# Kernel optimization log

Hardware: AMD Instinct MI355X
Metric: run time of the kernel (lower is better)

## Reference

```python
import jax, jax.numpy as jnp
import numpy as np

N_NODES = 50000
N_EDGES = 500000
IN_DIM = 64
OUT_DIM = 64
NUM_RELS = 16


def setup_inputs() -> dict:
    key = jax.random.key(0)
    ks = jax.random.split(key, 8)
    h = jax.random.normal(ks[0], (N_NODES, IN_DIM), dtype=jnp.float32)
    he = jax.random.normal(ks[1], (N_EDGES, IN_DIM), dtype=jnp.float32)
    src = jax.random.randint(ks[2], (N_EDGES,), 0, N_NODES)
    dst = jax.random.randint(ks[3], (N_EDGES,), 0, N_NODES)
    rel = jax.random.randint(ks[4], (N_EDGES,), 0, NUM_RELS)
    # xavier-ish scales
    W_shared = jax.random.normal(ks[5], (OUT_DIM, IN_DIM), dtype=jnp.float32) * (2.0 / (IN_DIM + OUT_DIM)) ** 0.5
    W_attn = jax.random.normal(ks[6], (1, 3 * OUT_DIM), dtype=jnp.float32) * (2.0 / (3 * OUT_DIM + 1)) ** 0.5
    W_rel = jax.random.normal(ks[7], (NUM_RELS, IN_DIM, OUT_DIM), dtype=jnp.float32) * (2.0 / (IN_DIM + OUT_DIM)) ** 0.5
    return {"h": h, "he": he, "src": src, "dst": dst, "rel": rel,
            "W_shared": W_shared, "W_attn": W_attn, "W_rel": W_rel}


def reference(h, he, src, dst, rel, W_shared, W_attn, W_rel):
    # --- edge attention: a = attn_fc([z_src, z_edge, z_dst]) (raw linear score, no softmax in original) ---
    Z = h @ W_shared.T                      # [N, out] project all nodes once
    ze = he @ W_shared.T                    # [E, out]
    # split attn weight to avoid materializing [E, 3*out] concat
    Wa_s, Wa_e, Wa_d = jnp.split(W_attn, 3, axis=1)   # each [1, out]
    a = Z[src] @ Wa_s.T + ze @ Wa_e.T + Z[dst] @ Wa_d.T   # [E, 1]
    # --- message: msg = (h_src @ W_rel[rel]) * a ---
    # compute per-(node, relation) transform once [N, R, out], then gather per edge
    H_all = jnp.einsum('ni,rio->nro', h, W_rel)          # [N, R, out]
    msg = H_all[src, rel] * a                             # [E, out]
    # --- scatter-sum aggregation into destination nodes ---
    out = jax.ops.segment_sum(msg, dst, num_segments=N_NODES)  # [N, out]
    # apply_func: activation (relu), no bias
    return jax.nn.relu(out)
```

## Files before the change

kernel.cpp:

```cpp
#include <hip/hip_runtime.h>
#include <math.h>

#define N_NODES 50000
#define N_EDGES 500000
#define NUM_RELS 16
#define GH 64
#define SCAN_BLKS 196
#define AE_BLKS 1954

typedef _Float16 f16x8 __attribute__((ext_vector_type(8)));
typedef _Float16 f16x4 __attribute__((ext_vector_type(4)));
typedef float    f32x4 __attribute__((ext_vector_type(4)));


__global__ void kz(int* __restrict__ c1, int* __restrict__ cu1,
                   int* __restrict__ c2, int* __restrict__ cu2) {
    int i = blockIdx.x * 256 + threadIdx.x;
    if (i < NUM_RELS) { c1[i] = 0; cu1[i] = 0; }
    if (i < N_NODES)  { c2[i] = 0; cu2[i] = 0; }
}

__global__ __launch_bounds__(256) void k_node(
    const float* __restrict__ h,
    const float* __restrict__ W_shared, const float* __restrict__ W_attn,
    const int* __restrict__ dst, const int* __restrict__ rel,
    float* __restrict__ sn, float* __restrict__ dn,
    int* __restrict__ c1, int* __restrict__ c2,
    _Float16* __restrict__ h_hi, _Float16* __restrict__ h_lo) {
    __shared__ float sus[64], sud[64];
    __shared__ int hist[NUM_RELS];
    const int t = threadIdx.x, bid = blockIdx.x, nb = gridDim.x;
    if (t < 64) {
        float us = 0.f, ud = 0.f;
        for (int o = 0; o < 64; ++o) {
            float w = W_shared[o * 64 + t];
            us = fmaf(w, W_attn[o],       us);
            ud = fmaf(w, W_attn[128 + o], ud);
        }
        sus[t] = us; sud[t] = ud;
    }
    if (t < NUM_RELS) hist[t] = 0;
    __syncthreads();

    int n = bid * 256 + t;
    if (n < N_NODES) {
        const float* hp = h + (size_t)n * 64;
        float s = 0.f, d = 0.f;
#pragma unroll
        for (int i = 0; i < 64; i += 4) {
            float4 v = *(const float4*)(hp + i);
            s = fmaf(v.x, sus[i], s);     s = fmaf(v.y, sus[i + 1], s);
            s = fmaf(v.z, sus[i + 2], s); s = fmaf(v.w, sus[i + 3], s);
            d = fmaf(v.x, sud[i], d);     d = fmaf(v.y, sud[i + 1], d);
            d = fmaf(v.z, sud[i + 2], d); d = fmaf(v.w, sud[i + 3], d);
            f16x4 hi, lo;
            hi[0] = (_Float16)v.x; lo[0] = (_Float16)(v.x - (float)hi[0]);
            hi[1] = (_Float16)v.y; lo[1] = (_Float16)(v.y - (float)hi[1]);
            hi[2] = (_Float16)v.z; lo[2] = (_Float16)(v.z - (float)hi[2]);
            hi[3] = (_Float16)v.w; lo[3] = (_Float16)(v.w - (float)hi[3]);
            *(f16x4*)(h_hi + (size_t)n * 64 + i) = hi;
            *(f16x4*)(h_lo + (size_t)n * 64 + i) = lo;
        }
        sn[n] = s; dn[n] = d;
    }
    for (int e = bid * 256 + t; e < N_EDGES; e += nb * 256) {
        atomicAdd(&hist[rel[e]], 1);
        atomicAdd(&c2[dst[e]], 1);
    }
    __syncthreads();
    if (t < NUM_RELS && hist[t]) atomicAdd(&c1[t], hist[t]);
}

__global__ __launch_bounds__(256) void k_scan1(const int* __restrict__ c2,
                                               int* __restrict__ partial) {
    const int t = threadIdx.x, bid = blockIdx.x;
    const int lane = t & 63, wv = t >> 6;
    __shared__ int ws[4];
    int idx = bid * 256 + t;
    int s = (idx < N_NODES) ? c2[idx] : 0;
#pragma unroll
    for (int off = 32; off > 0; off >>= 1) s += __shfl_xor(s, off, 64);
    if (lane == 0) ws[wv] = s;
    __syncthreads();
    if (t == 0) partial[bid] = ws[0] + ws[1] + ws[2] + ws[3];
}

__global__ __launch_bounds__(256) void k_scan2(const int* __restrict__ partial,
                                               int* __restrict__ pbase,
                                               int* __restrict__ offs2,
                                               const int* __restrict__ c1,
                                               int* __restrict__ offs1) {
    const int t = threadIdx.x;
    const int lane = t & 63, wv = t >> 6;
    __shared__ int wsum[4];
    int v = (t < SCAN_BLKS) ? partial[t] : 0;
    int x = v;
#pragma unroll
    for (int off = 1; off < 64; off <<= 1) {
        int y = __shfl_up(x, off, 64);
        if (lane >= off) x += y;
    }
    if (lane == 63) wsum[wv] = x;
    __syncthreads();
    int wbase = 0;
#pragma unroll
    for (int j = 0; j < 4; ++j) if (j < wv) wbase += wsum[j];
    int excl = wbase + x - v;
    pbase[t] = excl;
    if (t == 255) offs2[N_NODES] = excl;
    if (t == 0) {
        int b = 0;
        for (int r = 0; r < NUM_RELS; ++r) { offs1[r] = b; b += c1[r]; }
        offs1[NUM_RELS] = b;
    }
}

__global__ __launch_bounds__(256) void k_scan3(int* __restrict__ c2,
                                               const int* __restrict__ pbase,
                                               int* __restrict__ offs2) {
    const int t = threadIdx.x, bid = blockIdx.x;
    const int lane = t & 63, wv = t >> 6;
    __shared__ int wsum[4];
    int idx = bid * 256 + t;
    int v = (idx < N_NODES) ? c2[idx] : 0;
    int x = v;
#pragma unroll
    for (int off = 1; off < 64; off <<= 1) {
        int y = __shfl_up(x, off, 64);
        if (lane >= off) x += y;
    }
    if (lane == 63) wsum[wv] = x;
    __syncthreads();
    int wbase = 0;
#pragma unroll
    for (int j = 0; j < 4; ++j) if (j < wv) wbase += wsum[j];
    if (idx < N_NODES) offs2[idx] = pbase[bid] + wbase + x - v;
    if (idx < 4096) c2[idx] = 0;
}

__global__ __launch_bounds__(256) void k_ae(
    const float4* __restrict__ he4,
    const int* __restrict__ src, const int* __restrict__ dst,
    const int* __restrict__ rel,
    const float* __restrict__ W_shared, const float* __restrict__ W_attn,
    const float* __restrict__ sn, const float* __restrict__ dn,
    const int* __restrict__ offs1, int* __restrict__ cur1p,
    const int* __restrict__ offs2, int* __restrict__ cursor2,
    int* __restrict__ srcs, float* __restrict__ aes, int* __restrict__ perm) {
    __shared__ float sve[64];
    __shared__ float sdot[256];
    __shared__ int hist[NUM_RELS], bbase[NUM_RELS], soffs[NUM_RELS];
    const int t = threadIdx.x;
    const int lane = t & 63;
    const int w = t >> 6;
    const int e = blockIdx.x * 256 + t;

    const size_t fb = ((size_t)blockIdx.x * 256 + (size_t)w * 64) * 16;
    const size_t fmax = (size_t)N_EDGES * 16 - 1;
    float4 v[16];
#pragma unroll
    for (int k = 0; k < 16; ++k) {
        size_t fi = fb + (size_t)k * 64 + lane;
        if (fi > fmax) fi = fmax;
        v[k] = he4[fi];
    }

    if (t < 64) {
        float ve = 0.f;
        for (int o = 0; o < 64; ++o)
            ve = fmaf(W_shared[o * 64 + t], W_attn[64 + o], ve);
        sve[t] = ve;
    }
    if (t < NUM_RELS) { hist[t] = 0; soffs[t] = offs1[t]; }
    const bool valid = (e < N_EDGES);
    int r = 0, s_ = 0, d_ = 0;
    float sdv = 0.f;
    if (valid) {
        s_ = src[e]; d_ = dst[e]; r = rel[e];
        sdv = sn[s_] + dn[d_];
    }
    __syncthreads();

    {
        float4 u = *(const float4*)(sve + 4 * (lane & 15));
#pragma unroll
        for (int k = 0; k < 16; ++k) {
            float p = v[k].x * u.x + v[k].y * u.y + v[k].z * u.z + v[k].w * u.w;
            p += __shfl_xor(p, 1, 64);
            p += __shfl_xor(p, 2, 64);
            p += __shfl_xor(p, 4, 64);
            p += __shfl_xor(p, 8, 64);
            if ((lane & 15) == 0) sdot[w * 64 + k * 4 + (lane >> 4)] = p;
        }
    }
    int lpos = 0; float aev = 0.f;
    if (valid) {
        aev = sdot[t] + sdv;
        lpos = atomicAdd(&hist[r], 1);
    }
    __syncthreads();
    if (t < NUM_RELS) bbase[t] = hist[t] ? atomicAdd(&cur1p[t << 8], hist[t]) : 0;
    __syncthreads();
    if (valid) {
        int p1 = soffs[r] + bbase[r] + lpos;
        srcs[p1] = s_; aes[p1] = aev;
        int p2 = offs2[d_] + atomicAdd(&cursor2[d_], 1);
        perm[p1] = p2;
    }
}

__global__ __launch_bounds__(256, 4) void k_msg(
    const _Float16* __restrict__ h_hi, const _Float16* __restrict__ h_lo,
    const float* __restrict__ W_rel, const int* __restrict__ offs1,
    const int* __restrict__ srcs, const float* __restrict__ aes,
    const int* __restrict__ perm, float* __restrict__ msg)
{
    const int t = threadIdx.x;
    const int lane = t & 63;
    const int quad = lane >> 4;
    const int col  = lane & 15;
    const int wib  = t >> 6;
    const int rh   = blockIdx.x & 31;
    const int r    = rh & 15;
    const int half = rh >> 4;
    const int g    = blockIdx.x >> 5;
    const int wr   = g * 4 + wib;

    const int begin = __builtin_amdgcn_readfirstlane(offs1[r]);
    const int end   = __builtin_amdgcn_readfirstlane(offs1[r + 1]);

    const float* Wb = W_rel + (size_t)r * 4096;
    f16x8 bh[2][2], bl[2][2];
#pragma unroll
    for (int kb = 0; kb < 2; ++kb)
#pragma unroll
        for (int n2 = 0; n2 < 2; ++n2)
#pragma unroll
            for (int j = 0; j < 8; ++j) {
                float w = Wb[(kb * 32 + quad * 8 + j) * 64 + (half * 2 + n2) * 16 + col];
                _Float16 hi = (_Float16)w;
                bh[kb][n2][j] = hi;
                bl[kb][n2][j] = (_Float16)(w - (float)hi);
            }

    for (int base = begin + wr * 16; base < end; base += 256 * 16) {
        int m16 = end - base; if (m16 > 16) m16 = 16;
        const int ridx = base + (col < m16 ? col : m16 - 1);
        const int   sv = srcs[ridx];
        const float av = (col < m16) ? aes[ridx] : 0.f;
        const int   pv = (col < m16) ? perm[ridx] : 0;

        const _Float16* ph = h_hi + (size_t)sv * 64 + quad * 8;
        const _Float16* pl = h_lo + (size_t)sv * 64 + quad * 8;
        f16x8 ah0 = *(const f16x8*)ph, ah1 = *(const f16x8*)(ph + 32);
        f16x8 al0 = *(const f16x8*)pl, al1 = *(const f16x8*)(pl + 32);

        f32x4 acc0 = {0.f, 0.f, 0.f, 0.f};
        f32x4 acc1 = {0.f, 0.f, 0.f, 0.f};
        acc0 = __builtin_amdgcn_mfma_f32_16x16x32_f16(ah0, bh[0][0], acc0, 0, 0, 0);
        acc1 = __builtin_amdgcn_mfma_f32_16x16x32_f16(ah0, bh[0][1], acc1, 0, 0, 0);
        acc0 = __builtin_amdgcn_mfma_f32_16x16x32_f16(ah0, bl[0][0], acc0, 0, 0, 0);
        acc1 = __builtin_amdgcn_mfma_f32_16x16x32_f16(ah0, bl[0][1], acc1, 0, 0, 0);
        acc0 = __builtin_amdgcn_mfma_f32_16x16x32_f16(al0, bh[0][0], acc0, 0, 0, 0);
        acc1 = __builtin_amdgcn_mfma_f32_16x16x32_f16(al0, bh[0][1], acc1, 0, 0, 0);
        acc0 = __builtin_amdgcn_mfma_f32_16x16x32_f16(ah1, bh[1][0], acc0, 0, 0, 0);
        acc1 = __builtin_amdgcn_mfma_f32_16x16x32_f16(ah1, bh[1][1], acc1, 0, 0, 0);
        acc0 = __builtin_amdgcn_mfma_f32_16x16x32_f16(ah1, bl[1][0], acc0, 0, 0, 0);
        acc1 = __builtin_amdgcn_mfma_f32_16x16x32_f16(ah1, bl[1][1], acc1, 0, 0, 0);
        acc0 = __builtin_amdgcn_mfma_f32_16x16x32_f16(al1, bh[1][0], acc0, 0, 0, 0);
        acc1 = __builtin_amdgcn_mfma_f32_16x16x32_f16(al1, bh[1][1], acc1, 0, 0, 0);

#pragma unroll
        for (int reg = 0; reg < 4; ++reg) {
            const int m = quad * 4 + reg;
            const float am = __shfl(av, m, 64);
            const int   pm = __shfl(pv, m, 64);
            if (m < m16) {
                float* op = msg + (size_t)pm * 64 + half * 32 + col;
                op[0]  = am * acc0[reg];
                op[16] = am * acc1[reg];
            }
        }
    }
}

__global__ __launch_bounds__(256) void k_out(
    const float* __restrict__ msg,
    const int* __restrict__ offs2, float* __restrict__ out)
{
    const int lane = threadIdx.x & 63;
    const int gw   = blockIdx.x * 4 + (threadIdx.x >> 6);
    const int nw   = gridDim.x * 4;
    for (int n = gw; n < N_NODES; n += nw) {
        const int qb = offs2[n], qe = offs2[n + 1];
        float s0 = 0.f, s1 = 0.f, s2 = 0.f, s3 = 0.f;
        int q = qb;
        for (; q + 4 <= qe; q += 4) {
            s0 += msg[(size_t)q * 64 + lane];
            s1 += msg[(size_t)(q + 1) * 64 + lane];
            s2 += msg[(size_t)(q + 2) * 64 + lane];
            s3 += msg[(size_t)(q + 3) * 64 + lane];
        }
        for (; q < qe; ++q)
            s0 += msg[(size_t)q * 64 + lane];
        float s = (s0 + s1) + (s2 + s3);
        out[(size_t)n * 64 + lane] = fmaxf(s, 0.f);
    }
}

extern "C" void kernel_launch(void* const* d_in, const int* in_sizes, int n_in,
                              void* d_out, int out_size, void* d_ws, size_t ws_size,
                              hipStream_t stream) {
    const float*  h        = (const float*)d_in[0];
    const float4* he4      = (const float4*)d_in[1];
    const int*    src      = (const int*)d_in[2];
    const int*    dst      = (const int*)d_in[3];
    const int*    rel      = (const int*)d_in[4];
    const float*  W_shared = (const float*)d_in[5];
    const float*  W_attn   = (const float*)d_in[6];
    const float*  W_rel    = (const float*)d_in[7];
    float*        out      = (float*)d_out;

    int*      counts1 = (int*)d_ws + 0;
    int*      cursor1 = (int*)d_ws + 16;
    int*      offs1   = (int*)d_ws + 32;
    int*      counts2 = (int*)d_ws + 64;
    int*      cursor2 = (int*)d_ws + 50064;
    int*      offs2   = (int*)d_ws + 100064;
    float*    sn      = (float*)d_ws + 150080;
    float*    dn      = (float*)d_ws + 200080;
    int*      srcs    = (int*)d_ws + 250080;
    float*    aes     = (float*)d_ws + 750080;
    int*      perm    = (int*)d_ws + 1250080;
    _Float16* h_hi    = (_Float16*)((int*)d_ws + 1750080);
    _Float16* h_lo    = (_Float16*)((int*)d_ws + 3350080);
    int*      partial = srcs;
    int*      pbase   = srcs + 256;
    float*    msg     = (float*)d_in[1];

    kz<<<(N_NODES + 255) / 256, 256, 0, stream>>>(counts1, cursor1, counts2, cursor2);
    k_node<<<196, 256, 0, stream>>>(h, W_shared, W_attn, dst, rel,
                                    sn, dn, counts1, counts2, h_hi, h_lo);
    k_scan1<<<SCAN_BLKS, 256, 0, stream>>>(counts2, partial);
    k_scan2<<<1, 256, 0, stream>>>(partial, pbase, offs2, counts1, offs1);
    k_scan3<<<SCAN_BLKS, 256, 0, stream>>>(counts2, pbase, offs2);
    k_ae<<<AE_BLKS, 256, 0, stream>>>(he4, src, dst, rel, W_shared, W_attn, sn, dn,
                                      offs1, counts2, offs2, cursor2, srcs, aes, perm);
    k_msg<<<32 * GH, 256, 0, stream>>>(h_hi, h_lo, W_rel, offs1, srcs, aes, perm, msg);
    k_out<<<2048, 256, 0, stream>>>(msg, offs2, out);
}
```

Baseline: 337.8 us.

## Store messages in fp16 in relation order and gather via inverse permutation

The message kernel now writes per-edge messages as fp16, contiguously in relation-sorted order, instead of scattering fp32 rows to destination-sorted slots. The edge kernel records an inverse permutation (destination slot to relation slot), and the output kernel gathers message rows through it with an 8-way unrolled accumulation. This halves message write and read traffic and makes the message-kernel stores coalesced, in exchange for random row gathers in the reduction. It also adds fp16 rounding error to each message before summation.

```diff
diff --git a/kernel.cpp b/kernel.cpp
--- a/kernel.cpp
+++ b/kernel.cpp
@@ -146,7 +146,7 @@
     const float* __restrict__ sn, const float* __restrict__ dn,
     const int* __restrict__ offs1, int* __restrict__ cur1p,
     const int* __restrict__ offs2, int* __restrict__ cursor2,
-    int* __restrict__ srcs, float* __restrict__ aes, int* __restrict__ perm) {
+    int* __restrict__ srcs, float* __restrict__ aes, int* __restrict__ iperm) {
     __shared__ float sve[64];
     __shared__ float sdot[256];
     __shared__ int hist[NUM_RELS], bbase[NUM_RELS], soffs[NUM_RELS];
@@ -205,7 +205,7 @@
         int p1 = soffs[r] + bbase[r] + lpos;
         srcs[p1] = s_; aes[p1] = aev;
         int p2 = offs2[d_] + atomicAdd(&cursor2[d_], 1);
-        perm[p1] = p2;
+        iperm[p2] = p1;
     }
 }
 
@@ -213,7 +213,7 @@
     const _Float16* __restrict__ h_hi, const _Float16* __restrict__ h_lo,
     const float* __restrict__ W_rel, const int* __restrict__ offs1,
     const int* __restrict__ srcs, const float* __restrict__ aes,
-    const int* __restrict__ perm, float* __restrict__ msg)
+    _Float16* __restrict__ msg)
 {
     const int t = threadIdx.x;
     const int lane = t & 63;
@@ -248,7 +248,6 @@
         const int ridx = base + (col < m16 ? col : m16 - 1);
         const int   sv = srcs[ridx];
         const float av = (col < m16) ? aes[ridx] : 0.f;
-        const int   pv = (col < m16) ? perm[ridx] : 0;
 
         const _Float16* ph = h_hi + (size_t)sv * 64 + quad * 8;
         const _Float16* pl = h_lo + (size_t)sv * 64 + quad * 8;
@@ -274,18 +273,17 @@
         for (int reg = 0; reg < 4; ++reg) {
             const int m = quad * 4 + reg;
             const float am = __shfl(av, m, 64);
-            const int   pm = __shfl(pv, m, 64);
             if (m < m16) {
-                float* op = msg + (size_t)pm * 64 + half * 32 + col;
-                op[0]  = am * acc0[reg];
-                op[16] = am * acc1[reg];
+                _Float16* op = msg + (size_t)(base + m) * 64 + half * 32 + col;
+                op[0]  = (_Float16)(am * acc0[reg]);
+                op[16] = (_Float16)(am * acc1[reg]);
             }
         }
     }
 }
 
 __global__ __launch_bounds__(256) void k_out(
-    const float* __restrict__ msg,
+    const _Float16* __restrict__ msg, const int* __restrict__ iperm,
     const int* __restrict__ offs2, float* __restrict__ out)
 {
     const int lane = threadIdx.x & 63;
@@ -294,16 +292,30 @@
     for (int n = gw; n < N_NODES; n += nw) {
         const int qb = offs2[n], qe = offs2[n + 1];
         float s0 = 0.f, s1 = 0.f, s2 = 0.f, s3 = 0.f;
+        float s4 = 0.f, s5 = 0.f, s6 = 0.f, s7 = 0.f;
         int q = qb;
-        for (; q + 4 <= qe; q += 4) {
-            s0 += msg[(size_t)q * 64 + lane];
-            s1 += msg[(size_t)(q + 1) * 64 + lane];
-            s2 += msg[(size_t)(q + 2) * 64 + lane];
-            s3 += msg[(size_t)(q + 3) * 64 + lane];
-        }
-        for (; q < qe; ++q)
-            s0 += msg[(size_t)q * 64 + lane];
-        float s = (s0 + s1) + (s2 + s3);
+        for (; q + 8 <= qe; q += 8) {
+            int p0 = iperm[q],     p1 = iperm[q + 1];
+            int p2 = iperm[q + 2], p3 = iperm[q + 3];
+            int p4 = iperm[q + 4], p5 = iperm[q + 5];
+            int p6 = iperm[q + 6], p7 = iperm[q + 7];
+            s0 += (float)msg[(size_t)p0 * 64 + lane];
+            s1 += (float)msg[(size_t)p1 * 64 + lane];
+            s2 += (float)msg[(size_t)p2 * 64 + lane];
+            s3 += (float)msg[(size_t)p3 * 64 + lane];
+            s4 += (float)msg[(size_t)p4 * 64 + lane];
+            s5 += (float)msg[(size_t)p5 * 64 + lane];
+            s6 += (float)msg[(size_t)p6 * 64 + lane];
+            s7 += (float)msg[(size_t)p7 * 64 + lane];
+        }
+        for (; q + 2 <= qe; q += 2) {
+            int p0 = iperm[q], p1 = iperm[q + 1];
+            s0 += (float)msg[(size_t)p0 * 64 + lane];
+            s1 += (float)msg[(size_t)p1 * 64 + lane];
+        }
+        if (q < qe)
+            s0 += (float)msg[(size_t)iperm[q] * 64 + lane];
+        float s = ((s0 + s1) + (s2 + s3)) + ((s4 + s5) + (s6 + s7));
         out[(size_t)n * 64 + lane] = fmaxf(s, 0.f);
     }
 }
@@ -331,12 +343,12 @@
     float*    dn      = (float*)d_ws + 200080;
     int*      srcs    = (int*)d_ws + 250080;
     float*    aes     = (float*)d_ws + 750080;
-    int*      perm    = (int*)d_ws + 1250080;
+    int*      iperm   = (int*)d_ws + 1250080;
     _Float16* h_hi    = (_Float16*)((int*)d_ws + 1750080);
     _Float16* h_lo    = (_Float16*)((int*)d_ws + 3350080);
     int*      partial = srcs;
     int*      pbase   = srcs + 256;
-    float*    msg     = (float*)d_in[1];
+    _Float16* msg     = (_Float16*)d_in[1];
 
     kz<<<(N_NODES + 255) / 256, 256, 0, stream>>>(counts1, cursor1, counts2, cursor2);
     k_node<<<196, 256, 0, stream>>>(h, W_shared, W_attn, dst, rel,
@@ -345,7 +357,7 @@
     k_scan2<<<1, 256, 0, stream>>>(partial, pbase, offs2, counts1, offs1);
     k_scan3<<<SCAN_BLKS, 256, 0, stream>>>(counts2, pbase, offs2);
     k_ae<<<AE_BLKS, 256, 0, stream>>>(he4, src, dst, rel, W_shared, W_attn, sn, dn,
-                                      offs1, counts2, offs2, cursor2, srcs, aes, perm);
-    k_msg<<<32 * GH, 256, 0, stream>>>(h_hi, h_lo, W_rel, offs1, srcs, aes, perm, msg);
-    k_out<<<2048, 256, 0, stream>>>(msg, offs2, out);
-}
+                                      offs1, counts2, offs2, cursor2, srcs, aes, iperm);
+    k_msg<<<32 * GH, 256, 0, stream>>>(h_hi, h_lo, W_rel, offs1, srcs, aes, msg);
+    k_out<<<2048, 256, 0, stream>>>(msg, iperm, offs2, out);
+}
```

Measured after the change: 335.5 us. No clear change (-0.7%).
